# Kernel optimization log

Hardware: AMD Instinct MI355X
Metric: run time of the kernel (lower is better)

## Reference

```python
import jax, jax.numpy as jnp
import numpy as np

B, S, D, H = 4, 4096, 512, 8


def setup_inputs() -> dict:
    key = jax.random.key(0)
    ks = jax.random.split(key, 9)
    s = 1.0 / np.sqrt(D)
    return {
        "x": jax.random.normal(ks[0], (B, S, D), jnp.float32),
        "Wq": jax.random.normal(ks[1], (D, D), jnp.float32) * s,
        "bq": jax.random.normal(ks[2], (D,), jnp.float32) * 0.02,
        "Wk": jax.random.normal(ks[3], (D, D), jnp.float32) * s,
        "bk": jax.random.normal(ks[4], (D,), jnp.float32) * 0.02,
        "Wv": jax.random.normal(ks[5], (D, D), jnp.float32) * s,
        "bv": jax.random.normal(ks[6], (D,), jnp.float32) * 0.02,
        "Wo": jax.random.normal(ks[7], (H * D, D), jnp.float32) * (1.0 / np.sqrt(H * D)),
        "bo": jax.random.normal(ks[8], (D,), jnp.float32) * 0.02,
        "num_heads": H,
    }


def reference(x, Wq, bq, Wk, bk, Wv, bv, Wo, bo, num_heads):
    # Q/K/V projections (self-attention path; encoder_output=None)
    q = x @ Wq + bq  # [B,S,D]
    k = x @ Wk + bk
    v = x @ Wv + bv
    scale = 1.0 / jnp.sqrt(jnp.asarray(x.shape[-1], x.dtype))
    scores = jnp.einsum("bqd,bkd->bqk", q, k) * scale  # [B,S,S]
    probs = jax.nn.softmax(scores, axis=-1)
    attn = jnp.einsum("bqk,bkd->bqd", probs, v)  # [B,S,D]
    # Original stacks identical heads then torch.cat along dim=-1 -> tile H copies.
    cat = jnp.tile(attn, (1, 1, num_heads))  # [B,S,H*D]
    return cat @ Wo + bo  # [B,S,D]
```

## Files before the change

### kernel.cpp

```cpp
#include <hip/hip_runtime.h>
#include <stdint.h>

#define SCALE 0.04419417382415922f

typedef __bf16 bf16x8 __attribute__((ext_vector_type(8)));
typedef float f32x4 __attribute__((ext_vector_type(4)));
typedef uint16_t u16x8 __attribute__((ext_vector_type(8)));

static __device__ __forceinline__ uint16_t f2bf(float f) {
  union { float f; uint32_t u; } v; v.f = f;
  uint32_t u = v.u;
  return (uint16_t)((u + 0x7FFFu + ((u >> 16) & 1u)) >> 16);
}
static __device__ __forceinline__ float bf2f(uint16_t h) {
  union { uint32_t u; float f; } v; v.u = ((uint32_t)h) << 16;
  return v.f;
}

static __device__ __forceinline__ void gload16(const void* g, void* l) {
  __builtin_amdgcn_global_load_lds(
      (__attribute__((address_space(1))) void*)g,
      (__attribute__((address_space(3))) void*)l, 16, 0, 0);
}


__global__ __launch_bounds__(256)
void convert_x(const float* __restrict__ x, uint16_t* __restrict__ xb) {
  size_t i = ((size_t)blockIdx.x * 256 + threadIdx.x) * 8;
  float4 a = *(const float4*)(x + i);
  float4 b = *(const float4*)(x + i + 4);
  u16x8 o;
  o[0] = f2bf(a.x); o[1] = f2bf(a.y); o[2] = f2bf(a.z); o[3] = f2bf(a.w);
  o[4] = f2bf(b.x); o[5] = f2bf(b.y); o[6] = f2bf(b.z); o[7] = f2bf(b.w);
  *(u16x8*)(xb + i) = o;
}

__global__ __launch_bounds__(256)
void pack_w(const float* __restrict__ Wq, const float* __restrict__ Wk,
            const float* __restrict__ Wv, uint16_t* __restrict__ wt) {
  __shared__ float tile[64][65];
  const int k0 = blockIdx.x * 64, n0 = blockIdx.y * 64, m = blockIdx.z;
  const float* W = (m == 0) ? Wq : ((m == 1) ? Wk : Wv);
  const float scl = (m == 0) ? SCALE : 1.0f;
  const int t = threadIdx.x, r = t >> 2, c0 = (t & 3) * 16;
  #pragma unroll
  for (int j = 0; j < 4; j++) {
    float4 v = *(const float4*)&W[(size_t)(k0 + r) * 512 + n0 + c0 + j * 4];
    tile[r][c0 + j * 4 + 0] = v.x; tile[r][c0 + j * 4 + 1] = v.y;
    tile[r][c0 + j * 4 + 2] = v.z; tile[r][c0 + j * 4 + 3] = v.w;
  }
  __syncthreads();
  u16x8 o0, o1;
  #pragma unroll
  for (int e = 0; e < 8; e++) {
    o0[e] = f2bf(tile[c0 + e][r] * scl);
    o1[e] = f2bf(tile[c0 + 8 + e][r] * scl);
  }
  uint16_t* dst = wt + (size_t)(m * 512 + n0 + r) * 512 + k0 + c0;
  *(u16x8*)dst = o0;
  *(u16x8*)(dst + 8) = o1;
}

__global__ __launch_bounds__(256)
void pack_wo(const float* __restrict__ Wo, uint16_t* __restrict__ woT) {
  __shared__ float tile[64][65];
  const int k0 = blockIdx.x * 64, n0 = blockIdx.y * 64;
  const int t = threadIdx.x, r = t >> 2, c0 = (t & 3) * 16;
  float av[16];
  #pragma unroll
  for (int e = 0; e < 16; e++) av[e] = 0.f;
  for (int h = 0; h < 8; h++) {
    const float* src = &Wo[(size_t)(h * 512 + k0 + r) * 512 + n0 + c0];
    #pragma unroll
    for (int j = 0; j < 4; j++) {
      float4 v = *(const float4*)(src + j * 4);
      av[j * 4 + 0] += v.x; av[j * 4 + 1] += v.y;
      av[j * 4 + 2] += v.z; av[j * 4 + 3] += v.w;
    }
  }
  #pragma unroll
  for (int e = 0; e < 16; e++) tile[r][c0 + e] = av[e];
  __syncthreads();
  u16x8 o0, o1;
  #pragma unroll
  for (int e = 0; e < 8; e++) {
    o0[e] = f2bf(tile[c0 + e][r]);
    o1[e] = f2bf(tile[c0 + 8 + e][r]);
  }
  uint16_t* dst = woT + (size_t)(n0 + r) * 512 + k0 + c0;
  *(u16x8*)dst = o0;
  *(u16x8*)(dst + 8) = o1;
}

__global__ void pack_bias(const float* __restrict__ bq, const float* __restrict__ bk,
                          const float* __restrict__ bv, float* __restrict__ bqkv) {
  int i = blockIdx.x * 256 + threadIdx.x;
  if (i < 512) bqkv[i] = bq[i] * SCALE;
  else if (i < 1024) bqkv[i] = bk[i - 512];
  else if (i < 1536) bqkv[i] = bv[i - 1024];
}

__global__ __launch_bounds__(256)
void transpose_v(const uint16_t* __restrict__ qkv, uint16_t* __restrict__ Vt) {
  __shared__ uint16_t tile[64][72];
  const int s0 = blockIdx.x * 64, d0 = blockIdx.y * 64, b = blockIdx.z;
  const int t = threadIdx.x, r = t >> 2, c0 = (t & 3) * 16;
  const uint16_t* src = qkv + ((size_t)(b * 4096 + s0 + r)) * 1536 + 1024 + d0 + c0;
  *(u16x8*)&tile[r][c0] = *(const u16x8*)src;
  *(u16x8*)&tile[r][c0 + 8] = *(const u16x8*)(src + 8);
  __syncthreads();
  u16x8 o0, o1;
  #pragma unroll
  for (int e = 0; e < 8; e++) { o0[e] = tile[c0 + e][r]; o1[e] = tile[c0 + 8 + e][r]; }
  uint16_t* dst = Vt + ((size_t)b * 512 + d0 + r) * 4096 + s0 + c0;
  *(u16x8*)dst = o0;
  *(u16x8*)(dst + 8) = o1;
}

template<int MODE>
__global__ __launch_bounds__(256, 2)
void gemm2(const uint16_t* __restrict__ A, const uint16_t* __restrict__ Bt,
           const float* __restrict__ bias, void* __restrict__ Cout,
           float* __restrict__ sums,
           int M, int N, int K, int lda, int ldb, int ldc,
           long long aZ, long long bZ, long long cZ, long long sZ) {
  __shared__ __align__(16) uint16_t SH[16384];
  uint16_t* As = SH;
  uint16_t* Bs = SH + 8192;

  const int nbn = N >> 7;
  const int nwg = (M >> 7) * nbn;
  int id = blockIdx.x;
  id = (id & 7) * (nwg >> 3) + (id >> 3);
  const int bm = id / nbn, bn = id % nbn;
  const long long z = blockIdx.z;
  A += z * aZ; Bt += z * bZ;

  const int t = threadIdx.x;
  const int lane = t & 63, w = t >> 6;
  const int wr = w >> 1, wc = w & 1;
  const size_t m0 = (size_t)bm * 128, n0 = (size_t)bn * 128;

  f32x4 acc[4][4];
  #pragma unroll
  for (int i = 0; i < 4; i++)
    #pragma unroll
    for (int j = 0; j < 4; j++) acc[i][j] = (f32x4)(0.f);

  const uint16_t* ag = A + (m0 + (size_t)(t >> 2)) * lda + (t & 3) * 8;
  const uint16_t* bg = Bt + (n0 + (size_t)(t >> 2)) * ldb + (t & 3) * 8;

  auto stage = [&](int buf) {
    uint16_t* la = As + buf * 4096 + w * 512;
    uint16_t* lb = Bs + buf * 4096 + w * 512;
    gload16(ag, la);
    gload16(ag + (size_t)64 * lda, la + 2048);
    gload16(bg, lb);
    gload16(bg + (size_t)64 * ldb, lb + 2048);
    ag += 32; bg += 32;
  };
  auto compute = [&](int buf) {
    const uint16_t* pa = As + buf * 4096 + (wr * 64 + (lane & 15)) * 32 + (lane >> 4) * 8;
    const uint16_t* pb = Bs + buf * 4096 + (wc * 64 + (lane & 15)) * 32 + (lane >> 4) * 8;
    bf16x8 a[4], b[4];
    #pragma unroll
    for (int i = 0; i < 4; i++) a[i] = *(const bf16x8*)(pa + i * 512);
    #pragma unroll
    for (int i = 0; i < 4; i++) b[i] = *(const bf16x8*)(pb + i * 512);
    #pragma unroll
    for (int mi = 0; mi < 4; mi++)
      #pragma unroll
      for (int ni = 0; ni < 4; ni++)
        acc[mi][ni] = __builtin_amdgcn_mfma_f32_16x16x32_bf16(a[mi], b[ni], acc[mi][ni], 0, 0, 0);
  };

  int cur = 0;
  stage(0);
  asm volatile("s_waitcnt vmcnt(0)" ::: "memory");
  __builtin_amdgcn_s_barrier();
  __builtin_amdgcn_sched_barrier(0);
  const int iters = K >> 5;
  for (int it = 0; it < iters - 1; ++it) {
    stage(cur ^ 1);
    compute(cur);
    asm volatile("s_waitcnt vmcnt(0)" ::: "memory");
    __builtin_amdgcn_s_barrier();
    __builtin_amdgcn_sched_barrier(0);
    cur ^= 1;
  }
  compute(cur);

  const int g = lane >> 4, cl = lane & 15;
  const int crow = wr * 64 + g * 4;
  const int ccol = wc * 64 + cl;

  if (MODE == 1) {
    float bvv[4];
    #pragma unroll
    for (int ni = 0; ni < 4; ni++) bvv[ni] = bias[n0 + ccol + ni * 16];
    float* C = (float*)Cout + z * cZ;
    #pragma unroll
    for (int mi = 0; mi < 4; mi++)
      #pragma unroll
      for (int r = 0; r < 4; r++) {
        size_t gr = m0 + crow + mi * 16 + r;
        #pragma unroll
        for (int ni = 0; ni < 4; ni++)
          C[gr * (size_t)ldc + n0 + ccol + ni * 16] = acc[mi][ni][r] + bvv[ni];
      }
    return;
  }

  if (MODE == 2) {
    #pragma unroll
    for (int mi = 0; mi < 4; mi++)
      #pragma unroll
      for (int r = 0; r < 4; r++) {
        float s = 0.f;
        #pragma unroll
        for (int ni = 0; ni < 4; ni++) {
          float v = __expf(acc[mi][ni][r]);
          acc[mi][ni][r] = v;
          s += v;
        }
        s += __shfl_xor(s, 1); s += __shfl_xor(s, 2);
        s += __shfl_xor(s, 4); s += __shfl_xor(s, 8);
        if (cl == 0)
          sums[z * sZ + (m0 + crow + mi * 16 + r) * 64 + bn * 2 + wc] = s;
      }
  }

  float bvv[4];
  #pragma unroll
  for (int ni = 0; ni < 4; ni++)
    bvv[ni] = (MODE == 0) ? bias[n0 + ccol + ni * 16] : 0.f;
  float scl[4][4];
  if (MODE == 3) {
    #pragma unroll
    for (int mi = 0; mi < 4; mi++)
      #pragma unroll
      for (int r = 0; r < 4; r++)
        scl[mi][r] = sums[z * sZ + m0 + crow + mi * 16 + r];
  }

  uint16_t* C = (uint16_t*)Cout + z * cZ;
  #pragma unroll
  for (int h = 0; h < 2; ++h) {
    __syncthreads();
    if (wr == h) {
      #pragma unroll
      for (int mi = 0; mi < 4; mi++)
        #pragma unroll
        for (int r = 0; r < 4; r++) {
          const int lr = mi * 16 + g * 4 + r;
          #pragma unroll
          for (int ni = 0; ni < 4; ni++) {
            float v = acc[mi][ni][r] + bvv[ni];
            if (MODE == 3) v *= scl[mi][r];
            SH[lr * 136 + ccol + ni * 16] = f2bf(v);
          }
        }
    }
    __syncthreads();
    #pragma unroll
    for (int c = 0; c < 4; ++c) {
      const int idx = t + c * 256;
      const int row = idx >> 4, c8 = idx & 15;
      *(u16x8*)(C + (m0 + h * 64 + row) * (size_t)ldc + n0 + c8 * 8) =
          *(const u16x8*)(SH + row * 136 + c8 * 8);
    }
  }
}

__global__ __launch_bounds__(256)
void reduce_sums(const float* __restrict__ P, float* __restrict__ inv, int rows) {
  int r = blockIdx.x * 256 + threadIdx.x;
  if (r >= rows) return;
  const float4* p4 = (const float4*)(P + (size_t)r * 64);
  float s = 0.f;
  #pragma unroll
  for (int i = 0; i < 16; ++i) { float4 v = p4[i]; s += (v.x + v.y) + (v.z + v.w); }
  inv[r] = 1.f / s;
}


extern "C" void kernel_launch(void* const* d_in, const int* in_sizes, int n_in,
                              void* d_out, int out_size, void* d_ws, size_t ws_size,
                              hipStream_t stream) {
  const float* x   = (const float*)d_in[0];
  const float* Wq  = (const float*)d_in[1];
  const float* bq  = (const float*)d_in[2];
  const float* Wk  = (const float*)d_in[3];
  const float* bk  = (const float*)d_in[4];
  const float* Wv  = (const float*)d_in[5];
  const float* bvp = (const float*)d_in[6];
  const float* Wo  = (const float*)d_in[7];
  const float* bo  = (const float*)d_in[8];
  float* out = (float*)d_out;

  char* ws = (char*)d_ws;
  const size_t MB = (size_t)1 << 20;
  uint16_t* qkv   = (uint16_t*)(ws);
  uint16_t* Vt    = (uint16_t*)(ws + 48 * MB);
  uint16_t* attn  = (uint16_t*)(ws + 64 * MB);
  uint16_t* wqkvT = (uint16_t*)(ws + 80 * MB);
  uint16_t* woT   = (uint16_t*)(ws + 82 * MB);
  float*    bqkv  = (float*)   (ws + 83 * MB);
  float*    sumsP = (float*)   (ws + 84 * MB);
  float*    invs  = (float*)   (ws + 88 * MB);
  uint16_t* Sbuf  = (uint16_t*)(ws + 96 * MB);
  uint16_t* xb    = (uint16_t*)(ws + 96 * MB);

  const int nz = (ws_size >= 225 * MB) ? 4 : 2;

  convert_x<<<dim3(4096), dim3(256), 0, stream>>>(x, xb);
  pack_w<<<dim3(8, 8, 3), dim3(256), 0, stream>>>(Wq, Wk, Wv, wqkvT);
  pack_wo<<<dim3(8, 8), dim3(256), 0, stream>>>(Wo, woT);
  pack_bias<<<dim3(6), dim3(256), 0, stream>>>(bq, bk, bvp, bqkv);

  gemm2<0><<<dim3(1536, 1, 1), dim3(256), 0, stream>>>(
      xb, wqkvT, bqkv, qkv, nullptr,
      16384, 1536, 512, 512, 512, 1536, 0, 0, 0, 0);

  transpose_v<<<dim3(64, 8, 4), dim3(256), 0, stream>>>(qkv, Vt);

  for (int p = 0; p < 4 / nz; ++p) {
    const uint16_t* qb = qkv + (size_t)p * nz * 4096 * 1536;
    float* sp = sumsP + (size_t)p * nz * 4096 * 64;
    float* ip = invs + (size_t)p * nz * 4096;
    gemm2<2><<<dim3(1024, 1, nz), dim3(256), 0, stream>>>(
        qb, qb + 512, nullptr, Sbuf, sp,
        4096, 4096, 512, 1536, 1536, 4096,
        (long long)4096 * 1536, (long long)4096 * 1536, (long long)4096 * 4096,
        (long long)4096 * 64);
    reduce_sums<<<dim3(nz * 4096 / 256), dim3(256), 0, stream>>>(sp, ip, nz * 4096);
    gemm2<3><<<dim3(128, 1, nz), dim3(256), 0, stream>>>(
        Sbuf, Vt + (size_t)p * nz * 512 * 4096, nullptr,
        attn + (size_t)p * nz * 4096 * 512, ip,
        4096, 512, 4096, 4096, 4096, 512,
        (long long)4096 * 4096, (long long)512 * 4096, (long long)4096 * 512,
        4096);
  }

  gemm2<1><<<dim3(512, 1, 1), dim3(256), 0, stream>>>(
      attn, woT, bo, out, nullptr,
      16384, 512, 512, 512, 512, 512, 0, 0, 0, 0);
}
```

Measured before the change: 287.2 us.

## Replace 128x128 GEMM with 8-wave 256xBN kernel using swizzled LDS and interleaved pipeline

```diff
diff --git a/kernel.cpp b/kernel.cpp
--- a/kernel.cpp
+++ b/kernel.cpp
@@ -12,16 +12,16 @@
   uint32_t u = v.u;
   return (uint16_t)((u + 0x7FFFu + ((u >> 16) & 1u)) >> 16);
 }
-static __device__ __forceinline__ float bf2f(uint16_t h) {
-  union { uint32_t u; float f; } v; v.u = ((uint32_t)h) << 16;
-  return v.f;
-}
 
 static __device__ __forceinline__ void gload16(const void* g, void* l) {
   __builtin_amdgcn_global_load_lds(
       (__attribute__((address_space(1))) void*)g,
       (__attribute__((address_space(3))) void*)l, 16, 0, 0);
 }
+
+#define P_BAR asm volatile("s_barrier" ::: "memory")
+#define P_LGKM do { asm volatile("s_waitcnt lgkmcnt(0)" ::: "memory"); \
+                    __builtin_amdgcn_sched_barrier(0); } while (0)
 
 
 __global__ __launch_bounds__(256)
@@ -117,157 +117,221 @@
   *(u16x8*)(dst + 8) = o1;
 }
 
-template<int MODE>
-__global__ __launch_bounds__(256, 2)
-void gemm2(const uint16_t* __restrict__ A, const uint16_t* __restrict__ Bt,
+template<int BN, int MODE>
+__global__ __launch_bounds__(512, 2)
+void gemm8(const uint16_t* __restrict__ A, const uint16_t* __restrict__ Bt,
            const float* __restrict__ bias, void* __restrict__ Cout,
            float* __restrict__ sums,
            int M, int N, int K, int lda, int ldb, int ldc,
            long long aZ, long long bZ, long long cZ, long long sZ) {
-  __shared__ __align__(16) uint16_t SH[16384];
-  uint16_t* As = SH;
-  uint16_t* Bs = SH + 8192;
-
-  const int nbn = N >> 7;
-  const int nwg = (M >> 7) * nbn;
+  constexpr int NREP = BN / 64;
+  constexpr int NH = NREP / 2;
+  constexpr int WN = BN / 4;
+  constexpr int BELTS = BN * 64;
+  __shared__ uint16_t SH[32768 + 2 * BELTS];
+
+  const int nbn = N / BN;
+  const int nwg = (M >> 8) * nbn;
   int id = blockIdx.x;
   id = (id & 7) * (nwg >> 3) + (id >> 3);
   const int bm = id / nbn, bn = id % nbn;
   const long long z = blockIdx.z;
   A += z * aZ; Bt += z * bZ;
+  const size_t m0 = (size_t)bm * 256, n0 = (size_t)bn * BN;
 
   const int t = threadIdx.x;
   const int lane = t & 63, w = t >> 6;
-  const int wr = w >> 1, wc = w & 1;
-  const size_t m0 = (size_t)bm * 128, n0 = (size_t)bn * 128;
-
-  f32x4 acc[4][4];
-  #pragma unroll
-  for (int i = 0; i < 4; i++)
-    #pragma unroll
-    for (int j = 0; j < 4; j++) acc[i][j] = (f32x4)(0.f);
-
-  const uint16_t* ag = A + (m0 + (size_t)(t >> 2)) * lda + (t & 3) * 8;
-  const uint16_t* bg = Bt + (n0 + (size_t)(t >> 2)) * ldb + (t & 3) * 8;
-
-  auto stage = [&](int buf) {
-    uint16_t* la = As + buf * 4096 + w * 512;
-    uint16_t* lb = Bs + buf * 4096 + w * 512;
-    gload16(ag, la);
-    gload16(ag + (size_t)64 * lda, la + 2048);
-    gload16(bg, lb);
-    gload16(bg + (size_t)64 * ldb, lb + 2048);
-    ag += 32; bg += 32;
+  const int wr = w >> 2, wc = w & 3;
+  const int l15 = lane & 15, l4 = lane >> 4, l7 = lane & 7, l3 = lane >> 3;
+  const int sw = l7 ^ l3;
+
+  const uint16_t* srcA = A + (m0 + w * 8 + l3) * (size_t)lda + sw * 8;
+  const uint16_t* srcB = (BN == 256)
+      ? Bt + (n0 + (w >> 1) * 64 + (w & 1) * 16 + l3) * (size_t)ldb + sw * 8
+      : Bt + (n0 + (w >> 1) * 32 + (w & 1) * 8 + l3) * (size_t)ldb + sw * 8;
+
+  const int NKT = K >> 6;
+  const int NIT = NKT >> 1;
+
+  f32x4 acc[8][NREP];
+  #pragma unroll
+  for (int i = 0; i < 8; i++)
+    #pragma unroll
+    for (int j = 0; j < NREP; j++) acc[i][j] = (f32x4)(0.f);
+
+  bf16x8 a[4][2], b0[NH][2], b1[NH][2];
+
+  auto stageA = [&](int tile, int mh) {
+    const uint16_t* s = srcA + mh * 64 * (size_t)lda + tile * 64;
+    uint16_t* d = SH + (tile & 1) * 16384 + mh * 4096 + w * 512;
+    gload16(s, d);
+    gload16(s + 128 * (size_t)lda, d + 8192);
   };
-  auto compute = [&](int buf) {
-    const uint16_t* pa = As + buf * 4096 + (wr * 64 + (lane & 15)) * 32 + (lane >> 4) * 8;
-    const uint16_t* pb = Bs + buf * 4096 + (wc * 64 + (lane & 15)) * 32 + (lane >> 4) * 8;
-    bf16x8 a[4], b[4];
-    #pragma unroll
-    for (int i = 0; i < 4; i++) a[i] = *(const bf16x8*)(pa + i * 512);
-    #pragma unroll
-    for (int i = 0; i < 4; i++) b[i] = *(const bf16x8*)(pb + i * 512);
-    #pragma unroll
-    for (int mi = 0; mi < 4; mi++)
-      #pragma unroll
-      for (int ni = 0; ni < 4; ni++)
-        acc[mi][ni] = __builtin_amdgcn_mfma_f32_16x16x32_bf16(a[mi], b[ni], acc[mi][ni], 0, 0, 0);
+  auto stageB = [&](int tile, int nh) {
+    if (BN == 256) {
+      const uint16_t* s = srcB + nh * 32 * (size_t)ldb + tile * 64;
+      uint16_t* d = SH + 32768 + (tile & 1) * BELTS + (w >> 1) * 4096 + nh * 2048 + (w & 1) * 1024;
+      gload16(s, d);
+      gload16(s + 8 * (size_t)ldb, d + 512);
+    } else {
+      const uint16_t* s = srcB + nh * 16 * (size_t)ldb + tile * 64;
+      uint16_t* d = SH + 32768 + (tile & 1) * BELTS + (w >> 1) * 2048 + nh * 1024 + (w & 1) * 512;
+      gload16(s, d);
+    }
   };
-
-  int cur = 0;
-  stage(0);
+  auto loadA = [&](int buf, int mh) {
+    const uint16_t* base = SH + buf * 16384 + (wr * 128 + mh * 64 + l15) * 64;
+    #pragma unroll
+    for (int m = 0; m < 4; m++)
+      #pragma unroll
+      for (int ks = 0; ks < 2; ks++)
+        a[m][ks] = *(const bf16x8*)(base + m * 1024 + (((ks * 4 + l4) ^ l7) * 8));
+  };
+  auto loadB = [&](int buf, int nh, bf16x8 (&bd)[NH][2]) {
+    const uint16_t* base = SH + 32768 + buf * BELTS + (wc * WN + nh * (WN / 2) + l15) * 64;
+    #pragma unroll
+    for (int n = 0; n < NH; n++)
+      #pragma unroll
+      for (int ks = 0; ks < 2; ks++)
+        bd[n][ks] = *(const bf16x8*)(base + n * 1024 + (((ks * 4 + l4) ^ l7) * 8));
+  };
+  auto quad = [&](int mh, int nq, bf16x8 (&bq)[NH][2]) {
+    __builtin_amdgcn_s_setprio(1);
+    #pragma unroll
+    for (int m = 0; m < 4; m++)
+      #pragma unroll
+      for (int n = 0; n < NH; n++)
+        #pragma unroll
+        for (int ks = 0; ks < 2; ks++)
+          acc[mh * 4 + m][nq + n] = __builtin_amdgcn_mfma_f32_16x16x32_bf16(
+              a[m][ks], bq[n][ks], acc[mh * 4 + m][nq + n], 0, 0, 0);
+    __builtin_amdgcn_s_setprio(0);
+  };
+
+  stageA(0, 0); stageB(0, 0); stageA(0, 1); stageB(0, 1);
+  stageA(1, 0); stageB(1, 0); stageA(1, 1);
+  if (BN == 256) asm volatile("s_waitcnt vmcnt(6)" ::: "memory");
+  else           asm volatile("s_waitcnt vmcnt(5)" ::: "memory");
+  P_BAR;
+
+  for (int k = 0; k < NIT - 1; ++k) {
+    const int tt = 2 * k;
+    loadA(0, 0); loadB(0, 0, b0); stageB(tt + 1, 1);
+    P_BAR; P_LGKM; quad(0, 0, b0); P_BAR;
+    loadB(0, 1, b1); stageA(tt + 2, 0);
+    P_BAR; P_LGKM; quad(0, NH, b1); P_BAR;
+    loadA(0, 1); stageB(tt + 2, 0);
+    P_BAR; P_LGKM; quad(1, NH, b1); P_BAR;
+    stageA(tt + 2, 1);
+    if (BN == 256) asm volatile("s_waitcnt vmcnt(6)" ::: "memory");
+    else           asm volatile("s_waitcnt vmcnt(5)" ::: "memory");
+    P_BAR; quad(1, 0, b0); P_BAR;
+    loadA(1, 0); loadB(1, 0, b0); stageB(tt + 2, 1);
+    P_BAR; P_LGKM; quad(0, 0, b0); P_BAR;
+    loadB(1, 1, b1); stageA(tt + 3, 0);
+    P_BAR; P_LGKM; quad(0, NH, b1); P_BAR;
+    loadA(1, 1); stageB(tt + 3, 0);
+    P_BAR; P_LGKM; quad(1, NH, b1); P_BAR;
+    stageA(tt + 3, 1);
+    if (BN == 256) asm volatile("s_waitcnt vmcnt(6)" ::: "memory");
+    else           asm volatile("s_waitcnt vmcnt(5)" ::: "memory");
+    P_BAR; quad(1, 0, b0); P_BAR;
+  }
+  loadA(0, 0); loadB(0, 0, b0); stageB(NKT - 1, 1);
+  P_BAR; P_LGKM; quad(0, 0, b0); P_BAR;
+  loadB(0, 1, b1);
+  P_BAR; P_LGKM; quad(0, NH, b1); P_BAR;
+  loadA(0, 1);
+  P_BAR; P_LGKM; quad(1, NH, b1); P_BAR;
   asm volatile("s_waitcnt vmcnt(0)" ::: "memory");
-  __builtin_amdgcn_s_barrier();
-  __builtin_amdgcn_sched_barrier(0);
-  const int iters = K >> 5;
-  for (int it = 0; it < iters - 1; ++it) {
-    stage(cur ^ 1);
-    compute(cur);
-    asm volatile("s_waitcnt vmcnt(0)" ::: "memory");
-    __builtin_amdgcn_s_barrier();
-    __builtin_amdgcn_sched_barrier(0);
-    cur ^= 1;
-  }
-  compute(cur);
-
-  const int g = lane >> 4, cl = lane & 15;
-  const int crow = wr * 64 + g * 4;
-  const int ccol = wc * 64 + cl;
+  P_BAR; quad(1, 0, b0); P_BAR;
+  loadA(1, 0); loadB(1, 0, b0);
+  P_BAR; P_LGKM; quad(0, 0, b0); P_BAR;
+  loadB(1, 1, b1);
+  P_BAR; P_LGKM; quad(0, NH, b1); P_BAR;
+  loadA(1, 1);
+  P_BAR; P_LGKM; quad(1, NH, b1); P_BAR;
+  quad(1, 0, b0);
+
+  asm volatile("s_waitcnt vmcnt(0) lgkmcnt(0)" ::: "memory");
+  __syncthreads();
+
+  const int g = l4;
 
   if (MODE == 1) {
-    float bvv[4];
-    #pragma unroll
-    for (int ni = 0; ni < 4; ni++) bvv[ni] = bias[n0 + ccol + ni * 16];
+    float bvv[NREP];
+    #pragma unroll
+    for (int ni = 0; ni < NREP; ni++) bvv[ni] = bias[n0 + wc * WN + ni * 16 + l15];
     float* C = (float*)Cout + z * cZ;
     #pragma unroll
-    for (int mi = 0; mi < 4; mi++)
+    for (int am = 0; am < 8; am++)
       #pragma unroll
       for (int r = 0; r < 4; r++) {
-        size_t gr = m0 + crow + mi * 16 + r;
+        size_t gr = m0 + wr * 128 + am * 16 + g * 4 + r;
         #pragma unroll
-        for (int ni = 0; ni < 4; ni++)
-          C[gr * (size_t)ldc + n0 + ccol + ni * 16] = acc[mi][ni][r] + bvv[ni];
+        for (int ni = 0; ni < NREP; ni++)
+          C[gr * (size_t)ldc + n0 + wc * WN + ni * 16 + l15] = acc[am][ni][r] + bvv[ni];
       }
     return;
   }
 
   if (MODE == 2) {
     #pragma unroll
-    for (int mi = 0; mi < 4; mi++)
+    for (int am = 0; am < 8; am++)
       #pragma unroll
       for (int r = 0; r < 4; r++) {
         float s = 0.f;
         #pragma unroll
-        for (int ni = 0; ni < 4; ni++) {
-          float v = __expf(acc[mi][ni][r]);
-          acc[mi][ni][r] = v;
+        for (int ni = 0; ni < NREP; ni++) {
+          float v = __expf(acc[am][ni][r]);
+          acc[am][ni][r] = v;
           s += v;
         }
         s += __shfl_xor(s, 1); s += __shfl_xor(s, 2);
         s += __shfl_xor(s, 4); s += __shfl_xor(s, 8);
-        if (cl == 0)
-          sums[z * sZ + (m0 + crow + mi * 16 + r) * 64 + bn * 2 + wc] = s;
+        if (l15 == 0)
+          sums[z * sZ + (m0 + wr * 128 + am * 16 + g * 4 + r) * 64 + (n0 >> 6) + wc] = s;
       }
   }
 
-  float bvv[4];
-  #pragma unroll
-  for (int ni = 0; ni < 4; ni++)
-    bvv[ni] = (MODE == 0) ? bias[n0 + ccol + ni * 16] : 0.f;
-  float scl[4][4];
+  float bvv[NREP];
+  #pragma unroll
+  for (int ni = 0; ni < NREP; ni++)
+    bvv[ni] = (MODE == 0) ? bias[n0 + wc * WN + ni * 16 + l15] : 0.f;
+  float4 sc[8];
   if (MODE == 3) {
     #pragma unroll
-    for (int mi = 0; mi < 4; mi++)
-      #pragma unroll
-      for (int r = 0; r < 4; r++)
-        scl[mi][r] = sums[z * sZ + m0 + crow + mi * 16 + r];
-  }
-
-  uint16_t* C = (uint16_t*)Cout + z * cZ;
+    for (int am = 0; am < 8; am++)
+      sc[am] = *(const float4*)&sums[z * sZ + m0 + wr * 128 + am * 16 + g * 4];
+  }
+
+  constexpr int STR = BN + 8;
+  uint16_t* C16 = (uint16_t*)Cout + z * cZ;
   #pragma unroll
   for (int h = 0; h < 2; ++h) {
     __syncthreads();
     if (wr == h) {
       #pragma unroll
-      for (int mi = 0; mi < 4; mi++)
+      for (int am = 0; am < 8; am++)
         #pragma unroll
         for (int r = 0; r < 4; r++) {
-          const int lr = mi * 16 + g * 4 + r;
+          const int lr = am * 16 + g * 4 + r;
           #pragma unroll
-          for (int ni = 0; ni < 4; ni++) {
-            float v = acc[mi][ni][r] + bvv[ni];
-            if (MODE == 3) v *= scl[mi][r];
-            SH[lr * 136 + ccol + ni * 16] = f2bf(v);
+          for (int ni = 0; ni < NREP; ni++) {
+            float v = acc[am][ni][r] + bvv[ni];
+            if (MODE == 3) v *= ((const float*)&sc[am])[r];
+            SH[lr * STR + wc * WN + ni * 16 + l15] = f2bf(v);
           }
         }
     }
     __syncthreads();
-    #pragma unroll
-    for (int c = 0; c < 4; ++c) {
-      const int idx = t + c * 256;
-      const int row = idx >> 4, c8 = idx & 15;
-      *(u16x8*)(C + (m0 + h * 64 + row) * (size_t)ldc + n0 + c8 * 8) =
-          *(const u16x8*)(SH + row * 136 + c8 * 8);
+    constexpr int CPT = BN / 32;
+    #pragma unroll
+    for (int c = 0; c < CPT; ++c) {
+      const int idx = t + c * 512;
+      const int row = idx / (BN / 8), c8 = idx % (BN / 8);
+      *(u16x8*)(C16 + (m0 + h * 128 + row) * (size_t)ldc + n0 + c8 * 8) =
+          *(const u16x8*)(SH + row * STR + c8 * 8);
     }
   }
 }
@@ -318,7 +382,7 @@
   pack_wo<<<dim3(8, 8), dim3(256), 0, stream>>>(Wo, woT);
   pack_bias<<<dim3(6), dim3(256), 0, stream>>>(bq, bk, bvp, bqkv);
 
-  gemm2<0><<<dim3(1536, 1, 1), dim3(256), 0, stream>>>(
+  gemm8<256, 0><<<dim3(384, 1, 1), dim3(512), 0, stream>>>(
       xb, wqkvT, bqkv, qkv, nullptr,
       16384, 1536, 512, 512, 512, 1536, 0, 0, 0, 0);
 
@@ -328,13 +392,13 @@
     const uint16_t* qb = qkv + (size_t)p * nz * 4096 * 1536;
     float* sp = sumsP + (size_t)p * nz * 4096 * 64;
     float* ip = invs + (size_t)p * nz * 4096;
-    gemm2<2><<<dim3(1024, 1, nz), dim3(256), 0, stream>>>(
+    gemm8<256, 2><<<dim3(256, 1, nz), dim3(512), 0, stream>>>(
         qb, qb + 512, nullptr, Sbuf, sp,
         4096, 4096, 512, 1536, 1536, 4096,
         (long long)4096 * 1536, (long long)4096 * 1536, (long long)4096 * 4096,
         (long long)4096 * 64);
     reduce_sums<<<dim3(nz * 4096 / 256), dim3(256), 0, stream>>>(sp, ip, nz * 4096);
-    gemm2<3><<<dim3(128, 1, nz), dim3(256), 0, stream>>>(
+    gemm8<128, 3><<<dim3(64, 1, nz), dim3(512), 0, stream>>>(
         Sbuf, Vt + (size_t)p * nz * 512 * 4096, nullptr,
         attn + (size_t)p * nz * 4096 * 512, ip,
         4096, 512, 4096, 4096, 4096, 512,
@@ -342,7 +406,7 @@
         4096);
   }
 
-  gemm2<1><<<dim3(512, 1, 1), dim3(256), 0, stream>>>(
+  gemm8<128, 1><<<dim3(256, 1, 1), dim3(512), 0, stream>>>(
       attn, woT, bo, out, nullptr,
       16384, 512, 512, 512, 512, 512, 0, 0, 0, 0);
 }
```

New measurement: 272.1 us. 5.2% less time.
